# Kernel optimization log

Hardware: AMD Instinct MI355X
Metric: run time of the kernel (lower is better)

The kernel has to match this reference:

```python
import jax, jax.numpy as jnp
import numpy as np

EPS = 1e-5
B, C, H, W = 64, 256, 64, 64


def _masked_mean(p9, r0, r1, c0, c1):
    # p9: [B,3,3,9,H,W]; r0,r1: [B,3] int row bounds (per i); c0,c1: [B,3] int col bounds (per j)
    Hh, Ww = p9.shape[-2], p9.shape[-1]
    rows = jnp.arange(Hh, dtype=jnp.int32)
    cols = jnp.arange(Ww, dtype=jnp.int32)
    mr = (rows[None, None, :] >= r0[..., None]) & (rows[None, None, :] < r1[..., None])  # [B,3,H]
    mc = (cols[None, None, :] >= c0[..., None]) & (cols[None, None, :] < c1[..., None])  # [B,3,W]
    mask = (mr[:, :, None, :, None] & mc[:, None, :, None, :]).astype(p9.dtype)  # [B,3,3,H,W]
    cnt = mask.sum((-2, -1))  # [B,3,3]
    s = jnp.einsum('bijkhw,bijhw->bijk', p9, mask)
    return jnp.where(cnt[..., None] > 0, s / jnp.maximum(cnt, 1.0)[..., None], 0.0)  # [B,3,3,9]


def _subj_obj_bounds(bbox, Hh, Ww):
    # bbox: [B,4] = [y0,y1,x0,x1] normalized
    y0, y1, x0, x1 = bbox[:, 0], bbox[:, 1], bbox[:, 2], bbox[:, 3]
    ch = (y1 - y0) / 3.0
    cw = (x1 - x0) / 3.0
    idx = jnp.arange(3, dtype=bbox.dtype)
    r0 = jnp.floor(Hh * (y0[:, None] + idx * ch[:, None])).astype(jnp.int32)
    r1 = jnp.floor(Hh * (y0[:, None] + (idx + 1.0) * ch[:, None])).astype(jnp.int32)
    dr = r1 <= r0
    r1n = jnp.where(dr & (r1 < Hh - 1), r1 + 1, r1)
    r0n = jnp.where(dr & (r1 >= Hh - 1), r0 - 1, r0)
    c0 = jnp.floor(Ww * (x0[:, None] + idx * cw[:, None])).astype(jnp.int32)
    c1 = jnp.floor(Ww * (x0[:, None] + (idx + 1.0) * cw[:, None])).astype(jnp.int32)
    dc = c1 <= c0
    c1n = jnp.where(dc & (c1 < Ww), c1 + 1, c1)
    c0n = jnp.where(dc & (c1 >= Ww), c0 - 1, c0)
    return r0n, r1n, c0n, c1n


def _joint_bounds(bbox, bbox_s, bbox_o, Hh, Ww):
    # intersection of bbox with the 3x3 cells of union(bbox_s, bbox_o)
    uy0 = jnp.minimum(bbox_s[:, 0], bbox_o[:, 0])
    uy1 = jnp.maximum(bbox_s[:, 1], bbox_o[:, 1])
    ux0 = jnp.minimum(bbox_s[:, 2], bbox_o[:, 2])
    ux1 = jnp.maximum(bbox_s[:, 3], bbox_o[:, 3])
    ch = (uy1 - uy0) / 3.0
    cw = (ux1 - ux0) / 3.0
    idx = jnp.arange(3, dtype=bbox.dtype)
    ylo = uy0[:, None] + idx * ch[:, None]
    yhi = uy0[:, None] + (idx + 1.0) * ch[:, None]
    xlo = ux0[:, None] + idx * cw[:, None]
    xhi = ux0[:, None] + (idx + 1.0) * cw[:, None]
    r0 = jnp.floor(Hh * jnp.maximum(bbox[:, 0][:, None], ylo)).astype(jnp.int32)
    r1 = jnp.floor(Hh * jnp.minimum(bbox[:, 1][:, None], yhi)).astype(jnp.int32)
    c0 = jnp.floor(Ww * jnp.maximum(bbox[:, 2][:, None], xlo)).astype(jnp.int32)
    c1 = jnp.floor(Ww * jnp.minimum(bbox[:, 3][:, None], xhi)).astype(jnp.int32)
    return r0, r1, c0, c1


def setup_inputs() -> dict:
    key = jax.random.key(0)
    ks = jax.random.split(key, 16)
    feat = jax.random.normal(ks[0], (B, C, H, W), dtype=jnp.float32)

    def make_bbox(k):
        k1, k2, k3, k4 = jax.random.split(k, 4)
        y0 = jax.random.uniform(k1, (B,), minval=0.0, maxval=0.4)
        y1 = jnp.minimum(y0 + jax.random.uniform(k2, (B,), minval=0.3, maxval=0.55), 0.99)
        x0 = jax.random.uniform(k3, (B,), minval=0.0, maxval=0.4)
        x1 = jnp.minimum(x0 + jax.random.uniform(k4, (B,), minval=0.3, maxval=0.55), 0.99)
        return jnp.stack([y0, y1, x0, x1], axis=1).astype(jnp.float32)

    bbox_s = make_bbox(ks[1])
    bbox_o = make_bbox(ks[2])
    predicate = jax.random.uniform(ks[3], (B, 9), dtype=jnp.float32)
    conv_w = jax.random.normal(ks[4], (324, 256), dtype=jnp.float32) * 0.02
    conv_b = jax.random.normal(ks[5], (324,), dtype=jnp.float32) * 0.02
    bn2_g = jax.random.uniform(ks[6], (324,), minval=0.5, maxval=1.5)
    bn2_b = jax.random.normal(ks[7], (324,)) * 0.02
    bn2_m = jax.random.normal(ks[8], (324,)) * 0.02
    bn2_v = jax.random.uniform(ks[9], (324,), minval=0.5, maxval=1.5)
    fc1_w = jax.random.normal(ks[10], (40, 81), dtype=jnp.float32) * 0.1
    fc1_b = jnp.zeros((40,), jnp.float32)
    bn1_g = jax.random.uniform(ks[11], (40,), minval=0.5, maxval=1.5)
    bn1_b = jax.random.normal(ks[12], (40,)) * 0.02
    bn1_m = jax.random.normal(ks[13], (40,)) * 0.02
    bn1_v = jax.random.uniform(ks[14], (40,), minval=0.5, maxval=1.5)
    fc2_w = jax.random.normal(ks[15], (9, 40), dtype=jnp.float32) * 0.1
    fc2_b = jnp.zeros((9,), jnp.float32)
    return dict(feat=feat, bbox_s=bbox_s, bbox_o=bbox_o, predicate=predicate,
                conv_w=conv_w, conv_b=conv_b, bn2_g=bn2_g, bn2_b=bn2_b, bn2_m=bn2_m, bn2_v=bn2_v,
                fc1_w=fc1_w, fc1_b=fc1_b, bn1_g=bn1_g, bn1_b=bn1_b, bn1_m=bn1_m, bn1_v=bn1_v,
                fc2_w=fc2_w, fc2_b=fc2_b)


def reference(feat, bbox_s, bbox_o, predicate, conv_w, conv_b, bn2_g, bn2_b, bn2_m, bn2_v,
              fc1_w, fc1_b, bn1_g, bn1_b, bn1_m, bn1_v, fc2_w, fc2_b):
    # 1x1 conv 256 -> 324, then BatchNorm2d (inference mode)
    prs = jnp.einsum('bchw,oc->bohw', feat, conv_w) + conv_b[None, :, None, None]
    prs = (prs - bn2_m[None, :, None, None]) * (bn2_g / jnp.sqrt(bn2_v + EPS))[None, :, None, None] + bn2_b[None, :, None, None]
    Bb, _, Hh, Ww = prs.shape
    # channel layout: start = i*27 + j*9 + k  ->  reshape to [B,3,3,9,H,W]
    def bank(lo):
        return prs[:, lo:lo + 81].reshape(Bb, 3, 3, 9, Hh, Ww)
    prs_s, prs_o, prs_js, prs_jo = bank(0), bank(81), bank(162), bank(243)

    feature_s = _masked_mean(prs_s, *_subj_obj_bounds(bbox_s, Hh, Ww))
    feature_o = _masked_mean(prs_o, *_subj_obj_bounds(bbox_o, Hh, Ww))
    feature_j = (_masked_mean(prs_js, *_joint_bounds(bbox_s, bbox_s, bbox_o, Hh, Ww)) +
                 _masked_mean(prs_jo, *_joint_bounds(bbox_o, bbox_s, bbox_o, Hh, Ww)))

    f = feature_s + feature_o + feature_j            # [B,3,3,9]
    f = jnp.transpose(f, (0, 3, 1, 2)).reshape(Bb, 81)  # torch layout [B,9,3,3] flattened

    h = f @ fc1_w.T + fc1_b
    h = (h - bn1_m) * (bn1_g / jnp.sqrt(bn1_v + EPS)) + bn1_b
    logits = h @ fc2_w.T + fc2_b
    return jnp.sum(logits * predicate, axis=1)
```

## Files before the change

kernel.cpp:

```cpp
#include <hip/hip_runtime.h>
#include <hip/hip_bf16.h>
#include <cstdint>

#define BB 64
#define CC 256
#define EPSF 1e-5f
#define PLANES 4

__device__ __forceinline__ void region_bounds(int bank, int i, int j,
                                              float sy0, float sy1, float sx0, float sx1,
                                              float oy0, float oy1, float ox0, float ox1,
                                              int& r0, int& r1, int& c0, int& c1) {
    float fi = (float)i, fj = (float)j;
    if (bank < 2) {
        float y0 = bank ? oy0 : sy0, y1 = bank ? oy1 : sy1;
        float x0 = bank ? ox0 : sx0, x1 = bank ? ox1 : sx1;
        float ch = __fdiv_rn(__fsub_rn(y1, y0), 3.0f);
        float cw = __fdiv_rn(__fsub_rn(x1, x0), 3.0f);
        int R0 = (int)floorf(__fmul_rn(64.0f, __fadd_rn(y0, __fmul_rn(fi, ch))));
        int R1 = (int)floorf(__fmul_rn(64.0f, __fadd_rn(y0, __fmul_rn(__fadd_rn(fi, 1.0f), ch))));
        bool dr = (R1 <= R0);
        r1 = (dr && (R1 < 63)) ? R1 + 1 : R1;
        r0 = (dr && (R1 >= 63)) ? R0 - 1 : R0;
        int C0 = (int)floorf(__fmul_rn(64.0f, __fadd_rn(x0, __fmul_rn(fj, cw))));
        int C1 = (int)floorf(__fmul_rn(64.0f, __fadd_rn(x0, __fmul_rn(__fadd_rn(fj, 1.0f), cw))));
        bool dc = (C1 <= C0);
        c1 = (dc && (C1 < 64)) ? C1 + 1 : C1;
        c0 = (dc && (C1 >= 64)) ? C0 - 1 : C0;
    } else {
        float by0 = (bank == 2) ? sy0 : oy0, by1 = (bank == 2) ? sy1 : oy1;
        float bx0 = (bank == 2) ? sx0 : ox0, bx1 = (bank == 2) ? sx1 : ox1;
        float uy0 = fminf(sy0, oy0), uy1 = fmaxf(sy1, oy1);
        float ux0 = fminf(sx0, ox0), ux1 = fmaxf(sx1, ox1);
        float ch = __fdiv_rn(__fsub_rn(uy1, uy0), 3.0f);
        float cw = __fdiv_rn(__fsub_rn(ux1, ux0), 3.0f);
        float ylo = __fadd_rn(uy0, __fmul_rn(fi, ch));
        float yhi = __fadd_rn(uy0, __fmul_rn(__fadd_rn(fi, 1.0f), ch));
        float xlo = __fadd_rn(ux0, __fmul_rn(fj, cw));
        float xhi = __fadd_rn(ux0, __fmul_rn(__fadd_rn(fj, 1.0f), cw));
        r0 = (int)floorf(__fmul_rn(64.0f, fmaxf(by0, ylo)));
        r1 = (int)floorf(__fmul_rn(64.0f, fminf(by1, yhi)));
        c0 = (int)floorf(__fmul_rn(64.0f, fmaxf(bx0, xlo)));
        c1 = (int)floorf(__fmul_rn(64.0f, fminf(bx1, xhi)));
    }
}

__global__ __launch_bounds__(64) void k_region_sums(const float* __restrict__ feat,
                                                    const float* __restrict__ bbox_s,
                                                    const float* __restrict__ bbox_o,
                                                    float* __restrict__ M) {
    int blk = blockIdx.x;
    int l = threadIdx.x;
    int pid0 = blk * PLANES;
    int b = pid0 >> 8;

    float sy0 = bbox_s[b * 4 + 0], sy1 = bbox_s[b * 4 + 1];
    float sx0 = bbox_s[b * 4 + 2], sx1 = bbox_s[b * 4 + 3];
    float oy0 = bbox_o[b * 4 + 0], oy1 = bbox_o[b * 4 + 1];
    float ox0 = bbox_o[b * 4 + 2], ox1 = bbox_o[b * 4 + 3];

    int rl = 0, rh = 0, cl = 0, chh = 0;
    if (l < 36) {
        int bank = l / 9, ij = l % 9, i = ij / 3, j = ij % 3;
        int r0, r1, c0, c1;
        region_bounds(bank, i, j, sy0, sy1, sx0, sx1, oy0, oy1, ox0, ox1, r0, r1, c0, c1);
        rl = max(r0, 0); rh = min(r1, 64);
        cl = max(c0, 0); chh = min(c1, 64);
    }

    __shared__ float S[64 * 65];
    const float4* src = (const float4*)feat + (size_t)pid0 * 1024;

    float4 ra[16], rb[16];

#define LOADP(R, P)                                                         \
    {                                                                       \
        const float4* s2 = src + (size_t)(P) * 1024;                        \
        _Pragma("unroll")                                                   \
        for (int it = 0; it < 16; ++it) R[it] = s2[it * 64 + l];            \
    }

#define STOREP(R)                                                           \
    {                                                                       \
        _Pragma("unroll")                                                   \
        for (int it = 0; it < 16; ++it) {                                   \
            int f = it * 256 + l * 4;                                       \
            int h = f >> 6, w = f & 63;                                     \
            float* dst = &S[h * 65 + w];                                    \
            dst[0] = R[it].x; dst[1] = R[it].y;                             \
            dst[2] = R[it].z; dst[3] = R[it].w;                             \
        }                                                                   \
    }

#define ROWSCAN()                                                           \
    {                                                                       \
        float run = 0.0f; int base = l * 65;                                \
        _Pragma("unroll 16")                                                \
        for (int i = 0; i < 64; ++i) { run += S[base + i]; S[base + i] = run; } \
    }

#define COLSCAN()                                                           \
    {                                                                       \
        float run = 0.0f;                                                   \
        _Pragma("unroll 16")                                                \
        for (int i = 0; i < 64; ++i) { run += S[i * 65 + l]; S[i * 65 + l] = run; } \
    }

#define EVALP(P)                                                            \
    if (l < 36) {                                                           \
        float s = 0.0f;                                                     \
        if (rh > rl && chh > cl) {                                          \
            float a2 = S[(rh - 1) * 65 + (chh - 1)];                        \
            float q  = (cl > 0) ? S[(rh - 1) * 65 + (cl - 1)] : 0.0f;       \
            float pp = (rl > 0) ? S[(rl - 1) * 65 + (chh - 1)] : 0.0f;      \
            float dd = (rl > 0 && cl > 0) ? S[(rl - 1) * 65 + (cl - 1)] : 0.0f; \
            s = a2 - q - pp + dd;                                           \
        }                                                                   \
        M[((size_t)(pid0 + (P))) * 36 + l] = s;                             \
    }

#define PLANE(CUR, NXT, P, PREFETCH)                                        \
    __syncthreads();                                                        \
    STOREP(CUR);                                                            \
    __syncthreads();                                                        \
    if (PREFETCH) LOADP(NXT, (P) + 1);                                      \
    ROWSCAN();                                                              \
    __syncthreads();                                                        \
    COLSCAN();                                                              \
    __syncthreads();                                                        \
    EVALP(P);

    LOADP(ra, 0);
    PLANE(ra, rb, 0, 1);
    PLANE(rb, ra, 1, 1);
    PLANE(ra, rb, 2, 1);
    PLANE(rb, ra, 3, 0);

#undef LOADP
#undef STOREP
#undef ROWSCAN
#undef COLSCAN
#undef EVALP
#undef PLANE
}

__global__ __launch_bounds__(384) void k_head(const float* __restrict__ M,
                                              const float* __restrict__ bbox_s,
                                              const float* __restrict__ bbox_o,
                                              const float* __restrict__ conv_w,
                                              const float* __restrict__ conv_b,
                                              const float* __restrict__ g2,
                                              const float* __restrict__ b2,
                                              const float* __restrict__ m2,
                                              const float* __restrict__ v2,
                                              const float* __restrict__ fc1_w,
                                              const float* __restrict__ fc1_b,
                                              const float* __restrict__ g1,
                                              const float* __restrict__ b1,
                                              const float* __restrict__ m1,
                                              const float* __restrict__ v1,
                                              const float* __restrict__ fc2_w,
                                              const float* __restrict__ fc2_b,
                                              const float* __restrict__ pred,
                                              float* __restrict__ out) {
    int b = blockIdx.x;
    int t = threadIdx.x;

    __shared__ float Ml[256 * 37];
    __shared__ float val[324];
    __shared__ float fv[81];
    __shared__ float hv[40];
    __shared__ float lg[9];

    for (int i = t; i < 256 * 36; i += 384) {
        int c = i / 36, r = i - c * 36;
        Ml[c * 37 + r] = M[(size_t)b * (256 * 36) + i];
    }
    __syncthreads();

    if (t < 324) {
        int region = t / 9, k = t - region * 9;
        int bank = region / 9, ij = region - bank * 9;
        int ii = ij / 3, jj = ij % 3;
        int o = bank * 81 + ii * 27 + jj * 9 + k;

        float sy0 = bbox_s[b * 4 + 0], sy1 = bbox_s[b * 4 + 1];
        float sx0 = bbox_s[b * 4 + 2], sx1 = bbox_s[b * 4 + 3];
        float oy0 = bbox_o[b * 4 + 0], oy1 = bbox_o[b * 4 + 1];
        float ox0 = bbox_o[b * 4 + 2], ox1 = bbox_o[b * 4 + 3];
        int r0, r1, c0, c1;
        region_bounds(bank, ii, jj, sy0, sy1, sx0, sx1, oy0, oy1, ox0, ox1, r0, r1, c0, c1);
        int nrows = max(0, min(r1, 64) - max(r0, 0));
        int ncols = max(0, min(c1, 64) - max(c0, 0));
        float cnt = (float)(nrows * ncols);

        float v = 0.0f;
        if (cnt > 0.0f) {
            const float* w = conv_w + o * 256;
            float dot = 0.0f;
            #pragma unroll 8
            for (int c = 0; c < 256; ++c) dot += w[c] * Ml[c * 37 + region];
            float mean = dot / cnt;
            float sc = g2[o] / sqrtf(v2[o] + EPSF);
            v = (mean + conv_b[o] - m2[o]) * sc + b2[o];
        }
        val[region * 9 + k] = v;
    }
    __syncthreads();

    if (t < 81) {
        int k = t / 9, ij = t - k * 9;
        fv[t] = val[(0 + ij) * 9 + k] + val[(9 + ij) * 9 + k] +
                val[(18 + ij) * 9 + k] + val[(27 + ij) * 9 + k];
    }
    __syncthreads();

    if (t < 40) {
        float h = fc1_b[t];
        for (int u = 0; u < 81; ++u) h += fv[u] * fc1_w[t * 81 + u];
        h = (h - m1[t]) * (g1[t] / sqrtf(v1[t] + EPSF)) + b1[t];
        hv[t] = h;
    }
    __syncthreads();

    if (t < 9) {
        float lgt = fc2_b[t];
        for (int u = 0; u < 40; ++u) lgt += hv[u] * fc2_w[t * 40 + u];
        lg[t] = lgt * pred[b * 9 + t];
    }
    __syncthreads();

    if (t == 0) {
        float s = 0.0f;
        for (int i = 0; i < 9; ++i) s += lg[i];
        out[b] = s;
    }
}

extern "C" void kernel_launch(void* const* d_in, const int* in_sizes, int n_in,
                              void* d_out, int out_size, void* d_ws, size_t ws_size,
                              hipStream_t stream) {
    const float* feat   = (const float*)d_in[0];
    const float* bbox_s = (const float*)d_in[1];
    const float* bbox_o = (const float*)d_in[2];
    const float* pred   = (const float*)d_in[3];
    const float* conv_w = (const float*)d_in[4];
    const float* conv_b = (const float*)d_in[5];
    const float* g2     = (const float*)d_in[6];
    const float* b2     = (const float*)d_in[7];
    const float* m2     = (const float*)d_in[8];
    const float* v2     = (const float*)d_in[9];
    const float* fc1_w  = (const float*)d_in[10];
    const float* fc1_b  = (const float*)d_in[11];
    const float* g1     = (const float*)d_in[12];
    const float* b1     = (const float*)d_in[13];
    const float* m1     = (const float*)d_in[14];
    const float* v1     = (const float*)d_in[15];
    const float* fc2_w  = (const float*)d_in[16];
    const float* fc2_b  = (const float*)d_in[17];
    float* out = (float*)d_out;

    float* M = (float*)d_ws;

    k_region_sums<<<(BB * CC) / PLANES, 64, 0, stream>>>(feat, bbox_s, bbox_o, M);
    k_head<<<BB, 384, 0, stream>>>(M, bbox_s, bbox_o, conv_w, conv_b, g2, b2, m2, v2,
                                   fc1_w, fc1_b, g1, b1, m1, v1, fc2_w, fc2_b,
                                   pred, out);
}
```

Before: 65.06 us.

## Replace full 2D prefix scan with column scan at needed rows only

The region-sum kernel no longer builds a full 64x65 integral image per plane with row and column scans and four barriers. Each thread now scans one column in registers and stores only the running sums at the row boundaries actually needed, which are chosen by a wave-uniform bitmask of region row edges. Each region sum is then a loop over its columns subtracting two compacted rows. The head kernel transposes M into shared memory so the conv dot product can use float4 reads, and launch bounds add an occupancy hint. This cuts shared-memory traffic and barriers, but the per-region column loop is serial and the ZROW=24 slot limit assumes at most 24 distinct boundary rows.

Result: faster. 63.02 us (-3.1%).

```diff
diff --git a/kernel.cpp b/kernel.cpp
--- a/kernel.cpp
+++ b/kernel.cpp
@@ -6,6 +6,8 @@
 #define CC 256
 #define EPSF 1e-5f
 #define PLANES 4
+#define ZROW 24
+#define SSTR 65
 
 __device__ __forceinline__ void region_bounds(int bank, int i, int j,
                                               float sy0, float sy1, float sx0, float sx1,
@@ -45,13 +47,12 @@
     }
 }
 
-__global__ __launch_bounds__(64) void k_region_sums(const float* __restrict__ feat,
-                                                    const float* __restrict__ bbox_s,
-                                                    const float* __restrict__ bbox_o,
-                                                    float* __restrict__ M) {
-    int blk = blockIdx.x;
+__global__ __launch_bounds__(64, 4) void k_region_sums(const float* __restrict__ feat,
+                                                       const float* __restrict__ bbox_s,
+                                                       const float* __restrict__ bbox_o,
+                                                       float* __restrict__ M) {
     int l = threadIdx.x;
-    int pid0 = blk * PLANES;
+    int pid0 = blockIdx.x * PLANES;
     int b = pid0 >> 8;
 
     float sy0 = bbox_s[b * 4 + 0], sy1 = bbox_s[b * 4 + 1];
@@ -59,89 +60,73 @@
     float oy0 = bbox_o[b * 4 + 0], oy1 = bbox_o[b * 4 + 1];
     float ox0 = bbox_o[b * 4 + 2], ox1 = bbox_o[b * 4 + 3];
 
-    int rl = 0, rh = 0, cl = 0, chh = 0;
+    int myb = l / 9, myrest = l % 9, myi = myrest / 3, myj = myrest % 3;
+
+    unsigned long long rowmask = 0ull;
+    int my_r0c = 0, my_r1c = 0;
+    #pragma unroll
+    for (int bk = 0; bk < 4; ++bk) {
+        #pragma unroll
+        for (int i = 0; i < 3; ++i) {
+            int r0, r1, c0, c1;
+            region_bounds(bk, i, 0, sy0, sy1, sx0, sx1, oy0, oy1, ox0, ox1, r0, r1, c0, c1);
+            int r0c = max(r0, 0), r1c = min(r1, 64);
+            if (r1c >= 1) rowmask |= 1ull << (r1c - 1);
+            if (r0c >= 1) rowmask |= 1ull << (r0c - 1);
+            if (bk == myb && i == myi) { my_r0c = r0c; my_r1c = r1c; }
+        }
+    }
+    unsigned int mlo = __builtin_amdgcn_readfirstlane((unsigned int)rowmask);
+    unsigned int mhi = __builtin_amdgcn_readfirstlane((unsigned int)(rowmask >> 32));
+    unsigned long long smask = (((unsigned long long)mhi) << 32) | mlo;
+
+    int cl = 0, ch = 0, idx0 = ZROW, idx1 = ZROW;
     if (l < 36) {
-        int bank = l / 9, ij = l % 9, i = ij / 3, j = ij % 3;
         int r0, r1, c0, c1;
-        region_bounds(bank, i, j, sy0, sy1, sx0, sx1, oy0, oy1, ox0, ox1, r0, r1, c0, c1);
-        rl = max(r0, 0); rh = min(r1, 64);
-        cl = max(c0, 0); chh = min(c1, 64);
-    }
-
-    __shared__ float S[64 * 65];
-    const float4* src = (const float4*)feat + (size_t)pid0 * 1024;
-
-    float4 ra[16], rb[16];
-
-#define LOADP(R, P)                                                         \
-    {                                                                       \
-        const float4* s2 = src + (size_t)(P) * 1024;                        \
-        _Pragma("unroll")                                                   \
-        for (int it = 0; it < 16; ++it) R[it] = s2[it * 64 + l];            \
-    }
-
-#define STOREP(R)                                                           \
-    {                                                                       \
-        _Pragma("unroll")                                                   \
-        for (int it = 0; it < 16; ++it) {                                   \
-            int f = it * 256 + l * 4;                                       \
-            int h = f >> 6, w = f & 63;                                     \
-            float* dst = &S[h * 65 + w];                                    \
-            dst[0] = R[it].x; dst[1] = R[it].y;                             \
-            dst[2] = R[it].z; dst[3] = R[it].w;                             \
-        }                                                                   \
-    }
-
-#define ROWSCAN()                                                           \
-    {                                                                       \
-        float run = 0.0f; int base = l * 65;                                \
-        _Pragma("unroll 16")                                                \
-        for (int i = 0; i < 64; ++i) { run += S[base + i]; S[base + i] = run; } \
-    }
-
-#define COLSCAN()                                                           \
-    {                                                                       \
-        float run = 0.0f;                                                   \
-        _Pragma("unroll 16")                                                \
-        for (int i = 0; i < 64; ++i) { run += S[i * 65 + l]; S[i * 65 + l] = run; } \
-    }
-
-#define EVALP(P)                                                            \
-    if (l < 36) {                                                           \
-        float s = 0.0f;                                                     \
-        if (rh > rl && chh > cl) {                                          \
-            float a2 = S[(rh - 1) * 65 + (chh - 1)];                        \
-            float q  = (cl > 0) ? S[(rh - 1) * 65 + (cl - 1)] : 0.0f;       \
-            float pp = (rl > 0) ? S[(rl - 1) * 65 + (chh - 1)] : 0.0f;      \
-            float dd = (rl > 0 && cl > 0) ? S[(rl - 1) * 65 + (cl - 1)] : 0.0f; \
-            s = a2 - q - pp + dd;                                           \
-        }                                                                   \
-        M[((size_t)(pid0 + (P))) * 36 + l] = s;                             \
-    }
-
-#define PLANE(CUR, NXT, P, PREFETCH)                                        \
-    __syncthreads();                                                        \
-    STOREP(CUR);                                                            \
-    __syncthreads();                                                        \
-    if (PREFETCH) LOADP(NXT, (P) + 1);                                      \
-    ROWSCAN();                                                              \
-    __syncthreads();                                                        \
-    COLSCAN();                                                              \
-    __syncthreads();                                                        \
-    EVALP(P);
-
-    LOADP(ra, 0);
-    PLANE(ra, rb, 0, 1);
-    PLANE(rb, ra, 1, 1);
-    PLANE(ra, rb, 2, 1);
-    PLANE(rb, ra, 3, 0);
-
-#undef LOADP
-#undef STOREP
-#undef ROWSCAN
-#undef COLSCAN
-#undef EVALP
-#undef PLANE
+        region_bounds(myb, myi, myj, sy0, sy1, sx0, sx1, oy0, oy1, ox0, ox1, r0, r1, c0, c1);
+        cl = max(c0, 0); ch = min(c1, 64);
+        if (my_r1c <= my_r0c) {
+            ch = cl;
+        } else {
+            idx1 = __popcll(smask & ((1ull << (my_r1c - 1)) - 1ull));
+            idx0 = (my_r0c > 0) ? (int)__popcll(smask & ((1ull << (my_r0c - 1)) - 1ull)) : ZROW;
+        }
+    }
+
+    __shared__ float S[(ZROW + 1) * SSTR];
+    S[ZROW * SSTR + l] = 0.0f;
+    __syncthreads();
+
+    const float* pf = feat + (size_t)pid0 * 4096 + l;
+    for (int p = 0; p < PLANES; ++p) {
+        float x[32];
+        float run = 0.0f;
+        int slot = 0;
+        #pragma unroll
+        for (int h = 0; h < 32; ++h) x[h] = pf[h * 64];
+        #pragma unroll
+        for (int h = 0; h < 32; ++h) {
+            run += x[h];
+            if ((smask >> h) & 1ull) { S[slot * SSTR + l] = run; ++slot; }
+        }
+        #pragma unroll
+        for (int h = 0; h < 32; ++h) x[h] = pf[(32 + h) * 64];
+        #pragma unroll
+        for (int h = 0; h < 32; ++h) {
+            run += x[h];
+            if ((smask >> (32 + h)) & 1ull) { S[slot * SSTR + l] = run; ++slot; }
+        }
+        __syncthreads();
+
+        if (l < 36) {
+            float s = 0.0f;
+            for (int w = cl; w < ch; ++w)
+                s += S[idx1 * SSTR + w] - S[idx0 * SSTR + w];
+            M[(size_t)(pid0 + p) * 36 + l] = s;
+        }
+        __syncthreads();
+        pf += 4096;
+    }
 }
 
 __global__ __launch_bounds__(384) void k_head(const float* __restrict__ M,
@@ -166,15 +151,15 @@
     int b = blockIdx.x;
     int t = threadIdx.x;
 
-    __shared__ float Ml[256 * 37];
+    __shared__ float MlT[36 * 264];
     __shared__ float val[324];
     __shared__ float fv[81];
     __shared__ float hv[40];
     __shared__ float lg[9];
 
-    for (int i = t; i < 256 * 36; i += 384) {
-        int c = i / 36, r = i - c * 36;
-        Ml[c * 37 + r] = M[(size_t)b * (256 * 36) + i];
+    for (int i = t; i < 36 * 256; i += 384) {
+        int r = i >> 8, c = i & 255;
+        MlT[r * 264 + c] = M[(size_t)b * (256 * 36) + c * 36 + r];
     }
     __syncthreads();
 
@@ -196,10 +181,16 @@
 
         float v = 0.0f;
         if (cnt > 0.0f) {
-            const float* w = conv_w + o * 256;
-            float dot = 0.0f;
+            const float4* wv = (const float4*)(conv_w + o * 256);
+            const float4* mv = (const float4*)(&MlT[region * 264]);
+            float4 a4 = make_float4(0.f, 0.f, 0.f, 0.f);
             #pragma unroll 8
-            for (int c = 0; c < 256; ++c) dot += w[c] * Ml[c * 37 + region];
+            for (int c4 = 0; c4 < 64; ++c4) {
+                float4 wq = wv[c4], mq = mv[c4];
+                a4.x += wq.x * mq.x; a4.y += wq.y * mq.y;
+                a4.z += wq.z * mq.z; a4.w += wq.w * mq.w;
+            }
+            float dot = (a4.x + a4.y) + (a4.z + a4.w);
             float mean = dot / cnt;
             float sc = g2[o] / sqrtf(v2[o] + EPSF);
             v = (mean + conv_b[o] - m2[o]) * sc + b2[o];
```
